# Kernel optimization log

Measured on AMD Instinct MI355X. Metric: run time of the kernel, lower is better.

The kernel has to match this reference:

```python
import jax, jax.numpy as jnp
import numpy as np

NUM_STEPS = 50   # global num_steps in source
SCALE = 1000     # global scale in source (fc1 out / fc2 in)
SUBTHRESH = 0.5  # HeavisideBoxcar surrogate half-width
THRESH = 1.0     # firing threshold

@jax.custom_vjp
def heaviside_boxcar(x):
    # spike = H(x); surrogate grad = boxcar of half-width SUBTHRESH
    return (x >= 0.0).astype(x.dtype)

def _hb_fwd(x):
    return heaviside_boxcar(x), x

def _hb_bwd(x, g):
    return (g * (jnp.abs(x) < SUBTHRESH).astype(g.dtype),)

heaviside_boxcar.defvjp(_hb_fwd, _hb_bwd)


def setup_inputs() -> dict:
    key = jax.random.key(0)
    k1, k2, k3 = jax.random.split(key, 3)
    B = 1024
    x = jax.random.uniform(k1, (B, 784), dtype=jnp.float32)  # pixel intensities in [0,1]
    W1 = jax.random.normal(k2, (SCALE, 784), jnp.float32) / np.sqrt(784).astype(np.float32)
    W2 = jax.random.normal(k3, (100, SCALE), jnp.float32) / np.sqrt(SCALE).astype(np.float32)
    tau_0 = jnp.array([2.0], jnp.float32)       # sigmoid(2) ~ 0.88 decay
    tau_vector = jnp.array([2.0], jnp.float32)
    acc_tau = jnp.array([2.0], jnp.float32)
    return {"x": x, "W1": W1, "W2": W2, "tau_0": tau_0,
            "tau_vector": tau_vector, "acc_tau": acc_tau}


def reference(x, W1, W2, tau_0, tau_vector, acc_tau):
    B = x.shape[0]
    # snn.spikegen.rate: per-step Bernoulli(p=x) spikes, shape [T, B, 784]
    u = jax.random.uniform(jax.random.key(42), (NUM_STEPS, B, 784), dtype=x.dtype)
    x_spk = (u < x[None]).astype(x.dtype)

    decay_0 = jax.nn.sigmoid(tau_0[0])
    decay_v = jax.nn.sigmoid(tau_vector[0])
    acc_decay = jax.nn.sigmoid(acc_tau[0])

    h1_mem = jnp.full((B, SCALE), 0.5, x.dtype)
    h1_spk = jnp.zeros((B, SCALE), x.dtype)
    h2_mem = jnp.full((B, 100), 0.5, x.dtype)
    h2_spk = jnp.zeros((B, 100), x.dtype)
    acc = jnp.zeros((B, 10), x.dtype)

    def step(carry, xt):
        h1m, h1s, h2m, h2s, acc = carry
        # pPLIF: mem = mem*decay*(1-spk) + I ; spike = H(mem - thresh)
        h1m = h1m * decay_0 * (1.0 - h1s) + xt @ W1.T
        h1s = heaviside_boxcar(h1m - THRESH)
        h2m = h2m * decay_v * (1.0 - h2s) + h1s @ W2.T
        h2s = heaviside_boxcar(h2m - THRESH)
        boost = jnp.mean(h2s.reshape(B, 10, 10), axis=2)  # AvgPool1d(10,10)
        acc = acc * acc_decay + boost                      # pPLI accumulator
        return (h1m, h1s, h2m, h2s, acc), None

    carry, _ = jax.lax.scan(step, (h1_mem, h1_spk, h2_mem, h2_spk, acc),
                            x_spk[:NUM_STEPS - 1])
    # torch loop runs under no_grad with detach(): block grads through it
    h1m, h1s, h2m, h2s, acc = jax.tree_util.tree_map(jax.lax.stop_gradient, carry)

    # final, differentiable step
    h1m = h1m * decay_0 * (1.0 - h1s) + x_spk[NUM_STEPS - 1] @ W1.T
    h1s = heaviside_boxcar(h1m - THRESH)
    h2m = h2m * decay_v * (1.0 - h2s) + h1s @ W2.T
    h2s = heaviside_boxcar(h2m - THRESH)
    boost = jnp.mean(h2s.reshape(B, 10, 10), axis=2)
    acc = acc * acc_decay + boost
    return acc
```

## Files before the change

### kernel.cpp

```cpp
#include <hip/hip_runtime.h>
#include <hip/hip_bf16.h>
#include <math.h>


#define NSTEPS 50
#define KC1 25
#define NSL 5

typedef __attribute__((ext_vector_type(4)))  int i32x4;
typedef __attribute__((ext_vector_type(16))) int i32x16;

#define OFF_B1     0ull
#define OFF_B2     5111808ull
#define OFF_H1MST  5898240ull
#define OFF_H1SST  14286848ull
#define OFF_H2MST  15335424ull
#define OFF_H2SST  16384000ull
#define OFF_ACCST  16515072ull
#define OFF_AF     16596992ull
#define FIXED_END  59195392ull
#define PERSTEP    8388608ull

#define PREP_BLOCKS 19200

__device__ __forceinline__ unsigned int rotl32(unsigned int v, int d) {
#if __has_builtin(__builtin_amdgcn_alignbit)
  return __builtin_amdgcn_alignbit(v, v, (unsigned int)(32 - d));
#else
  return (v << d) | (v >> (32 - d));
#endif
}

__device__ __forceinline__ unsigned int tf_bits(unsigned int i) {
  const unsigned int ks0 = 0u;
  const unsigned int ks1 = 42u;
  const unsigned int ks2 = 0x1BD11BDAu ^ 0u ^ 42u;
  unsigned int x0 = 0u + ks0;
  unsigned int x1 = i + ks1;
#define TF_RND(r) { x0 += x1; x1 = rotl32(x1, r); x1 ^= x0; }
  TF_RND(13) TF_RND(15) TF_RND(26) TF_RND(6)
  x0 += ks1; x1 += ks2 + 1u;
  TF_RND(17) TF_RND(29) TF_RND(16) TF_RND(24)
  x0 += ks2; x1 += ks0 + 2u;
  TF_RND(13) TF_RND(15) TF_RND(26) TF_RND(6)
  x0 += ks0; x1 += ks1 + 3u;
  TF_RND(17) TF_RND(29) TF_RND(16) TF_RND(24)
  x0 += ks1; x1 += ks2 + 4u;
  TF_RND(13) TF_RND(15) TF_RND(26) TF_RND(6)
  x0 += ks2; x1 += ks0 + 5u;
#undef TF_RND
  return x0 ^ x1;
}

__device__ __forceinline__ void spike_block(
    const float* __restrict__ x, i32x4* __restrict__ A, int t0, int gblk,
    int tid) {
  int g = gblk * 4 + (tid >> 6);
  int lane = tid & 63;
  int kc = g % 25;
  int r = g / 25;
  int mt = r & 31;
  int t = t0 + (r >> 5);
  int b = mt * 32 + (lane & 31);
  int j0 = kc * 32 + ((lane >> 5) << 4);
  unsigned int wds[4] = {0u, 0u, 0u, 0u};
  if (j0 < 784) {
    unsigned int base = (unsigned int)(t * 1024 + b) * 784u + (unsigned int)j0;
    const float* xp = x + b * 784 + j0;
#pragma unroll
    for (int q = 0; q < 4; ++q) {
      float4 xv = *(const float4*)(xp + 4 * q);
      unsigned int K0 = (unsigned int)(int)ceilf(xv.x * 8388608.0f);
      unsigned int K1 = (unsigned int)(int)ceilf(xv.y * 8388608.0f);
      unsigned int K2 = (unsigned int)(int)ceilf(xv.z * 8388608.0f);
      unsigned int K3 = (unsigned int)(int)ceilf(xv.w * 8388608.0f);
      unsigned int w4 = 0u;
      if ((tf_bits(base + 4 * q + 0) >> 9) < K0) w4 |= 1u;
      if ((tf_bits(base + 4 * q + 1) >> 9) < K1) w4 |= 1u << 8;
      if ((tf_bits(base + 4 * q + 2) >> 9) < K2) w4 |= 1u << 16;
      if ((tf_bits(base + 4 * q + 3) >> 9) < K3) w4 |= 1u << 24;
      wds[q] = w4;
    }
  }
  i32x4 v;
  v.x = (int)wds[0]; v.y = (int)wds[1]; v.z = (int)wds[2]; v.w = (int)wds[3];
  A[(size_t)(((t * 32 + mt) * 26) + kc) * 64 + lane] = v;
}

__global__ __launch_bounds__(256) void setup_kernel(
    const float* __restrict__ W1, const float* __restrict__ W2,
    signed char* __restrict__ B1, signed char* __restrict__ B2,
    const float* __restrict__ x, i32x4* __restrict__ A) {
  if (blockIdx.x >= PREP_BLOCKS) {
    spike_block(x, A, 0, blockIdx.x - PREP_BLOCKS, threadIdx.x);
    return;
  }
  int idx = blockIdx.x * 256 + threadIdx.x;
  const int NB1 = NSL * 32 * 26 * 1024;
  const int NB2 = NSL * 4 * 32 * 1024;
  float w;
  int s;
  signed char* dst;
  if (idx < NB1) {
    int jj = idx & 15;
    int lane = (idx >> 4) & 63;
    int kc = (idx >> 10) % 26;
    int rest = (idx >> 10) / 26;
    int nt = rest & 31;
    s = rest >> 5;
    int k = kc * 32 + ((lane >> 5) << 4) + jj;
    int o = nt * 32 + (lane & 31);
    w = (o < 1000 && k < 784) ? W1[o * 784 + k] : 0.0f;
    dst = B1 + idx;
  } else {
    int m = idx - NB1;
    if (m >= NB2) return;
    int jj = m & 15;
    int lane = (m >> 4) & 63;
    int kc = (m >> 10) & 31;
    int rest = (m >> 10) >> 5;
    int nt = rest & 3;
    s = rest >> 2;
    int k = kc * 32 + ((lane >> 5) << 4) + jj;
    int o = nt * 32 + (lane & 31);
    w = (o < 100 && k < 1000) ? W2[o * 1000 + k] : 0.0f;
    dst = B2 + m;
  }
  long long V = llrint((double)w * 281474976710656.0);
  signed char d = 0;
  for (int q = 0; q <= s + 1; ++q) {
    d = (signed char)(V & 0xFF);
    V = (V - (long long)d) >> 8;
  }
  *dst = d;
}

__global__ __launch_bounds__(256, 2) void gemm1_kernel(
    const signed char* __restrict__ Bf, const signed char* __restrict__ Afc,
    int* __restrict__ T1L, short* __restrict__ T1H) {
  __shared__ i32x4 bls[2][NSL][64];
  int tid = threadIdx.x, lane = tid & 63, wv = tid >> 6;
  int id = blockIdx.x;
  int low5 = id & 31;
  int nt = ((low5 & 7) << 2) | ((low5 >> 3) & 3);
  int mg = id >> 5;
  int tl = mg >> 2;
  int q  = mg & 3;
  int mtA = q * 8 + wv * 2;
  const i32x4* ApA = (const i32x4*)Afc + (size_t)((tl * 32 + mtA) * 26) * 64 + lane;
  const i32x4* ApB = ApA + 26 * 64;
  const i32x4* Bp = (const i32x4*)Bf + lane;
#define B1_IDX(s, kc) ((size_t)(((s) * 32 + nt) * 26 + (kc)) * 64)
  const bool st4 = (wv == 0);

  i32x16 CA[NSL], CB[NSL];
#pragma unroll
  for (int s = 0; s < NSL; ++s)
#pragma unroll
    for (int i = 0; i < 16; ++i) { CA[s][i] = 0; CB[s][i] = 0; }

  i32x4 sa = Bp[B1_IDX(wv, 0)];
  i32x4 sb; if (st4) sb = Bp[B1_IDX(4, 0)];
  i32x4 aA0 = ApA[0], aB0 = ApB[0];
  i32x4 aA1 = ApA[64], aB1 = ApB[64];
  i32x4 aA2, aB2;
  bls[0][wv][lane] = sa;
  if (st4) bls[0][4][lane] = sb;
  sa = Bp[B1_IDX(wv, 1)];
  if (st4) sb = Bp[B1_IDX(4, 1)];
  __syncthreads();

  for (int kc = 0; kc < KC1; ++kc) {
    const int cur = kc & 1, nxt = cur ^ 1;
    if (kc + 1 < KC1) {
      bls[nxt][wv][lane] = sa;
      if (st4) bls[nxt][4][lane] = sb;
    }
    if (kc + 2 < KC1) {
      sa = Bp[B1_IDX(wv, kc + 2)];
      if (st4) sb = Bp[B1_IDX(4, kc + 2)];
      aA2 = ApA[(size_t)(kc + 2) * 64];
      aB2 = ApB[(size_t)(kc + 2) * 64];
    }
#pragma unroll
    for (int s = 0; s < NSL; ++s) {
      i32x4 b = bls[cur][s][lane];
      CA[s] = __builtin_amdgcn_mfma_i32_32x32x32_i8(aA0, b, CA[s], 0, 0, 0);
      CB[s] = __builtin_amdgcn_mfma_i32_32x32x32_i8(aB0, b, CB[s], 0, 0, 0);
    }
    __syncthreads();
    aA0 = aA1; aA1 = aA2;
    aB0 = aB1; aB1 = aB2;
  }

  int o = nt * 32 + (lane & 31);
  int rb = 4 * (lane >> 5);
#pragma unroll
  for (int r = 0; r < 16; ++r) {
    int row = (r & 3) + 8 * (r >> 2) + rb;
    long long TA = (long long)CA[4][r];
    TA = (TA << 8) + (long long)CA[3][r];
    TA = (TA << 8) + (long long)CA[2][r];
    TA = (TA << 8) + (long long)CA[1][r];
    TA = (TA << 8) + (long long)CA[0][r];
    long long TB = (long long)CB[4][r];
    TB = (TB << 8) + (long long)CB[3][r];
    TB = (TB << 8) + (long long)CB[2][r];
    TB = (TB << 8) + (long long)CB[1][r];
    TB = (TB << 8) + (long long)CB[0][r];
    int bA = mtA * 32 + row;
    size_t i0 = ((size_t)tl * 1024 + bA) * 1024 + o;
    size_t i1 = ((size_t)tl * 1024 + bA + 32) * 1024 + o;
    T1L[i0] = (int)TA;
    T1H[i0] = (short)(TA >> 32);
    T1L[i1] = (int)TB;
    T1H[i1] = (short)(TB >> 32);
  }
}

__global__ __launch_bounds__(256) void rec1_kernel(
    const int* __restrict__ T1L, const short* __restrict__ T1H,
    signed char* __restrict__ h1sc,
    double* __restrict__ h1m_st, signed char* __restrict__ h1s_st,
    const float* __restrict__ tau0, int t0, int C,
    const float* __restrict__ x, i32x4* __restrict__ A, int t1) {
  if (blockIdx.x >= 512) {
    spike_block(x, A, t1, blockIdx.x - 512, threadIdx.x);
    return;
  }
  int tid = threadIdx.x;
  int lane = tid & 63, sub = tid >> 6;
  int b = blockIdx.x * 2 + (sub >> 1);
  int obase = (sub & 1) * 512 + lane;
  double alpha = 1.0 / (1.0 + exp(-(double)tau0[0]));
  double m[8], s[8];
  if (t0 == 0) {
#pragma unroll
    for (int j = 0; j < 8; ++j) { m[j] = 0.5; s[j] = 0.0; }
  } else {
#pragma unroll
    for (int j = 0; j < 8; ++j) {
      m[j] = h1m_st[(size_t)b * 1024 + obase + 64 * j];
      s[j] = (double)h1s_st[(size_t)b * 1024 + obase + 64 * j];
    }
  }
  for (int tl = 0; tl < C; ++tl) {
    const int*   Lp = T1L + ((size_t)tl * 1024 + b) * 1024 + obase;
    const short* Hp = T1H + ((size_t)tl * 1024 + b) * 1024 + obase;
    signed char* Sp = h1sc + ((size_t)tl * 1024 + b) * 1024 + obase;
#pragma unroll
    for (int j = 0; j < 8; ++j) {
      long long T = ((long long)Hp[64 * j] << 32) +
                    (long long)(unsigned int)Lp[64 * j];
      double I = (double)T * 0x1p-40;
      m[j] = (s[j] != 0.0 ? 0.0 : m[j] * alpha) + I;
      bool sp = (m[j] - 1.0) >= 0.0;
      s[j] = sp ? 1.0 : 0.0;
      Sp[64 * j] = sp ? 1 : 0;
    }
  }
#pragma unroll
  for (int j = 0; j < 8; ++j) {
    h1m_st[(size_t)b * 1024 + obase + 64 * j] = m[j];
    h1s_st[(size_t)b * 1024 + obase + 64 * j] = (signed char)(s[j] != 0.0 ? 1 : 0);
  }
}

__global__ __launch_bounds__(256, 3) void gemm2_kernel(
    const signed char* __restrict__ Bf, const signed char* __restrict__ h1sc,
    double* __restrict__ T2, int ngemm,
    const float* __restrict__ x, i32x4* __restrict__ A, int t1, int gofs) {
  if ((int)blockIdx.x >= ngemm) {
    spike_block(x, A, t1, gofs + (int)blockIdx.x - ngemm, threadIdx.x);
    return;
  }
  __shared__ i32x4 bls[2][NSL][64];
  int tid = threadIdx.x, lane = tid & 63, wv = tid >> 6;
  int nt = blockIdx.x & 3;
  int mg = blockIdx.x >> 2;
  int tl = mg >> 3;
  int mt = ((mg & 7) << 2) + wv;
  const signed char* Arow =
      h1sc + ((size_t)tl * 1024 + mt * 32 + (lane & 31)) * 1024 + ((lane >> 5) << 4);
  const i32x4* Bp = (const i32x4*)Bf + lane;
  const bool st4 = (wv == 0);
#define B2_IDX(s, kc) ((size_t)(((s) * 4 + nt) * 32 + (kc)) * 64)

  i32x16 C[NSL];
#pragma unroll
  for (int s = 0; s < NSL; ++s)
#pragma unroll
    for (int i = 0; i < 16; ++i) C[s][i] = 0;

  i32x4 sa = Bp[B2_IDX(wv, 0)];
  i32x4 sb; if (st4) sb = Bp[B2_IDX(4, 0)];
  i32x4 a0 = *(const i32x4*)(Arow);
  i32x4 a1 = *(const i32x4*)(Arow + 32);
  i32x4 a2;
  bls[0][wv][lane] = sa;
  if (st4) bls[0][4][lane] = sb;
  sa = Bp[B2_IDX(wv, 1)];
  if (st4) sb = Bp[B2_IDX(4, 1)];
  __syncthreads();

  for (int kc = 0; kc < 32; ++kc) {
    const int cur = kc & 1, nxt = cur ^ 1;
    if (kc + 1 < 32) {
      bls[nxt][wv][lane] = sa;
      if (st4) bls[nxt][4][lane] = sb;
    }
    if (kc + 2 < 32) {
      sa = Bp[B2_IDX(wv, kc + 2)];
      if (st4) sb = Bp[B2_IDX(4, kc + 2)];
      a2 = *(const i32x4*)(Arow + (size_t)(kc + 2) * 32);
    }
    i32x4 b0 = bls[cur][0][lane], b1 = bls[cur][1][lane], b2 = bls[cur][2][lane];
    i32x4 b3 = bls[cur][3][lane], b4 = bls[cur][4][lane];
    C[0] = __builtin_amdgcn_mfma_i32_32x32x32_i8(a0, b0, C[0], 0, 0, 0);
    C[1] = __builtin_amdgcn_mfma_i32_32x32x32_i8(a0, b1, C[1], 0, 0, 0);
    C[2] = __builtin_amdgcn_mfma_i32_32x32x32_i8(a0, b2, C[2], 0, 0, 0);
    C[3] = __builtin_amdgcn_mfma_i32_32x32x32_i8(a0, b3, C[3], 0, 0, 0);
    C[4] = __builtin_amdgcn_mfma_i32_32x32x32_i8(a0, b4, C[4], 0, 0, 0);
    a0 = a1; a1 = a2;
    __syncthreads();
  }

  int o = nt * 32 + (lane & 31);
  int rb = 4 * (lane >> 5);
#pragma unroll
  for (int r = 0; r < 16; ++r) {
    int row = (r & 3) + 8 * (r >> 2) + rb;
    int b = mt * 32 + row;
    long long T = (long long)C[4][r];
    T = (T << 8) + (long long)C[3][r];
    T = (T << 8) + (long long)C[2][r];
    T = (T << 8) + (long long)C[1][r];
    T = (T << 8) + (long long)C[0][r];
    T2[((size_t)tl * 1024 + b) * 128 + o] = (double)T * 0x1p-40;
  }
}

__global__ __launch_bounds__(256) void rec2_kernel(
    const double* __restrict__ T2, double* __restrict__ h2m_st,
    signed char* __restrict__ h2s_st, double* __restrict__ acc_st,
    const float* __restrict__ tauv, const float* __restrict__ acct,
    int t0, int C, float* __restrict__ out) {
  __shared__ signed char sp[256];
  int tid = threadIdx.x;
  int b = blockIdx.x * 2 + (tid >> 7);
  int o = tid & 127;
  double alpha = 1.0 / (1.0 + exp(-(double)tauv[0]));
  double adec  = 1.0 / (1.0 + exp(-(double)acct[0]));
  double m, s, accv = 0.0;
  bool isPool = (o < 10);
  if (t0 == 0) {
    m = 0.5; s = 0.0;
  } else {
    m = h2m_st[(size_t)b * 128 + o];
    s = (double)h2s_st[(size_t)b * 128 + o];
    if (isPool) accv = acc_st[b * 10 + o];
  }
  for (int tl = 0; tl < C; ++tl) {
    double I = T2[((size_t)tl * 1024 + b) * 128 + o];
    m = (s != 0.0 ? 0.0 : m * alpha) + I;
    bool spk = (m - 1.0) >= 0.0;
    s = spk ? 1.0 : 0.0;
    sp[tid] = spk ? 1 : 0;
    __syncthreads();
    if (isPool) {
      int base = tid & 128;
      int isum = 0;
#pragma unroll
      for (int k = 0; k < 10; ++k) isum += sp[base + o * 10 + k];
      accv = accv * adec + (double)isum / 10.0;
      if (t0 + tl == NSTEPS - 1) out[b * 10 + o] = (float)accv;
    }
    __syncthreads();
  }
  h2m_st[(size_t)b * 128 + o] = m;
  h2s_st[(size_t)b * 128 + o] = (signed char)(s != 0.0 ? 1 : 0);
  if (isPool) acc_st[b * 10 + o] = accv;
}

extern "C" void kernel_launch(void* const* d_in, const int* in_sizes, int n_in,
                              void* d_out, int out_size, void* d_ws, size_t ws_size,
                              hipStream_t stream) {
  const float* x    = (const float*)d_in[0];
  const float* W1   = (const float*)d_in[1];
  const float* W2   = (const float*)d_in[2];
  const float* tau0 = (const float*)d_in[3];
  const float* tauv = (const float*)d_in[4];
  const float* acct = (const float*)d_in[5];
  float* out = (float*)d_out;
  char*  ws  = (char*)d_ws;

  signed char* B1     = (signed char*)(ws + OFF_B1);
  signed char* B2     = (signed char*)(ws + OFF_B2);
  double*      h1m_st = (double*)(ws + OFF_H1MST);
  signed char* h1s_st = (signed char*)(ws + OFF_H1SST);
  double*      h2m_st = (double*)(ws + OFF_H2MST);
  signed char* h2s_st = (signed char*)(ws + OFF_H2SST);
  double*      acc_st = (double*)(ws + OFF_ACCST);
  signed char* Af     = (signed char*)(ws + OFF_AF);
  i32x4*       Afv    = (i32x4*)Af;

  long long avail = (long long)ws_size - (long long)FIXED_END;
  int C = (int)(avail / (long long)PERSTEP);
  if (C < 1) C = 1;
  if (C > 13) C = 13;
  size_t off_t1l  = FIXED_END;
  size_t off_t1h  = off_t1l + (size_t)C * 4194304ull;
  size_t off_h1sc = off_t1h + (size_t)C * 2097152ull;
  size_t off_t2   = off_h1sc + (size_t)C * 1048576ull;
  int*         T1L  = (int*)(ws + off_t1l);
  short*       T1H  = (short*)(ws + off_t1h);
  signed char* h1sc = (signed char*)(ws + off_h1sc);
  double*      T2   = (double*)(ws + off_t2);

  int C0 = (C < NSTEPS) ? C : NSTEPS;
  setup_kernel<<<PREP_BLOCKS + C0 * 200, 256, 0, stream>>>(
      W1, W2, B1, B2, x, Afv);

  for (int t0 = 0; t0 < NSTEPS; t0 += C) {
    int Cc = (NSTEPS - t0 < C) ? (NSTEPS - t0) : C;
    int t1 = t0 + Cc;
    int Cn = (t1 < NSTEPS) ? ((NSTEPS - t1 < C) ? (NSTEPS - t1) : C) : 0;
    int spkTot = Cn * 200;
    int spkA = spkTot / 2;
    int spkB = spkTot - spkA;
    int ngemm2 = 4 * Cc * 8;

    gemm1_kernel<<<32 * Cc * 4, 256, 0, stream>>>(
        B1, Af + (size_t)t0 * 851968ull, T1L, T1H);
    rec1_kernel<<<512 + spkA, 256, 0, stream>>>(
        T1L, T1H, h1sc, h1m_st, h1s_st, tau0, t0, Cc, x, Afv, t1);
    gemm2_kernel<<<ngemm2 + spkB, 256, 0, stream>>>(
        B2, h1sc, T2, ngemm2, x, Afv, t1, spkA);
    rec2_kernel<<<512, 256, 0, stream>>>(
        T2, h2m_st, h2s_st, acc_st, tauv, acct, t0, Cc, out);
  }
}
```

Measured before the change: 484.6 us.

## Preload whole W1 tile into LDS and drop per-chunk barriers in gemm1

Reorders the packed B1 weight layout so that each output tile's slices and k-chunks are contiguous. gemm1 then copies the whole 25x5 chunk set for its tile into shared memory (about 125 KB) once at the start. The main k-loop has no barriers or double-buffer stores, and A-operand prefetch now runs three chunks ahead. The larger LDS footprint forces occupancy down to one block per CU (launch bounds changed to 1), and the upfront bulk load is no longer overlapped with MFMA work.

```diff
diff --git a/kernel.cpp b/kernel.cpp
--- a/kernel.cpp
+++ b/kernel.cpp
@@ -104,10 +104,10 @@
   if (idx < NB1) {
     int jj = idx & 15;
     int lane = (idx >> 4) & 63;
-    int kc = (idx >> 10) % 26;
-    int rest = (idx >> 10) / 26;
-    int nt = rest & 31;
-    s = rest >> 5;
+    int fr = idx >> 10;
+    s = fr % 5;
+    int kc = (fr / 5) % 26;
+    int nt = fr / (5 * 26);
     int k = kc * 32 + ((lane >> 5) << 4) + jj;
     int o = nt * 32 + (lane & 31);
     w = (o < 1000 && k < 784) ? W1[o * 784 + k] : 0.0f;
@@ -135,10 +135,10 @@
   *dst = d;
 }
 
-__global__ __launch_bounds__(256, 2) void gemm1_kernel(
+__global__ __launch_bounds__(256, 1) void gemm1_kernel(
     const signed char* __restrict__ Bf, const signed char* __restrict__ Afc,
     int* __restrict__ T1L, short* __restrict__ T1H) {
-  __shared__ i32x4 bls[2][NSL][64];
+  __shared__ i32x4 bls[KC1 * NSL * 64];
   int tid = threadIdx.x, lane = tid & 63, wv = tid >> 6;
   int id = blockIdx.x;
   int low5 = id & 31;
@@ -147,11 +147,16 @@
   int tl = mg >> 2;
   int q  = mg & 3;
   int mtA = q * 8 + wv * 2;
+
+  const i32x4* Bg = (const i32x4*)Bf + (size_t)nt * (26 * NSL * 64);
+#pragma unroll
+  for (int i = 0; i < 32; ++i) {
+    int e = tid + 256 * i;
+    if (e < KC1 * NSL * 64) bls[e] = Bg[e];
+  }
+
   const i32x4* ApA = (const i32x4*)Afc + (size_t)((tl * 32 + mtA) * 26) * 64 + lane;
   const i32x4* ApB = ApA + 26 * 64;
-  const i32x4* Bp = (const i32x4*)Bf + lane;
-#define B1_IDX(s, kc) ((size_t)(((s) * 32 + nt) * 26 + (kc)) * 64)
-  const bool st4 = (wv == 0);
 
   i32x16 CA[NSL], CB[NSL];
 #pragma unroll
@@ -159,38 +164,26 @@
 #pragma unroll
     for (int i = 0; i < 16; ++i) { CA[s][i] = 0; CB[s][i] = 0; }
 
-  i32x4 sa = Bp[B1_IDX(wv, 0)];
-  i32x4 sb; if (st4) sb = Bp[B1_IDX(4, 0)];
-  i32x4 aA0 = ApA[0], aB0 = ApB[0];
-  i32x4 aA1 = ApA[64], aB1 = ApB[64];
-  i32x4 aA2, aB2;
-  bls[0][wv][lane] = sa;
-  if (st4) bls[0][4][lane] = sb;
-  sa = Bp[B1_IDX(wv, 1)];
-  if (st4) sb = Bp[B1_IDX(4, 1)];
   __syncthreads();
 
+  i32x4 aA0 = ApA[0],   aB0 = ApB[0];
+  i32x4 aA1 = ApA[64],  aB1 = ApB[64];
+  i32x4 aA2 = ApA[128], aB2 = ApB[128];
+
   for (int kc = 0; kc < KC1; ++kc) {
-    const int cur = kc & 1, nxt = cur ^ 1;
-    if (kc + 1 < KC1) {
-      bls[nxt][wv][lane] = sa;
-      if (st4) bls[nxt][4][lane] = sb;
-    }
-    if (kc + 2 < KC1) {
-      sa = Bp[B1_IDX(wv, kc + 2)];
-      if (st4) sb = Bp[B1_IDX(4, kc + 2)];
-      aA2 = ApA[(size_t)(kc + 2) * 64];
-      aB2 = ApB[(size_t)(kc + 2) * 64];
-    }
-#pragma unroll
-    for (int s = 0; s < NSL; ++s) {
-      i32x4 b = bls[cur][s][lane];
-      CA[s] = __builtin_amdgcn_mfma_i32_32x32x32_i8(aA0, b, CA[s], 0, 0, 0);
-      CB[s] = __builtin_amdgcn_mfma_i32_32x32x32_i8(aB0, b, CB[s], 0, 0, 0);
-    }
-    __syncthreads();
+    i32x4 ua = aA0, ub = aB0;
     aA0 = aA1; aA1 = aA2;
     aB0 = aB1; aB1 = aB2;
+    if (kc + 3 < KC1) {
+      aA2 = ApA[(size_t)(kc + 3) * 64];
+      aB2 = ApB[(size_t)(kc + 3) * 64];
+    }
+#pragma unroll
+    for (int s = 0; s < NSL; ++s) {
+      i32x4 b = bls[(kc * NSL + s) * 64 + lane];
+      CA[s] = __builtin_amdgcn_mfma_i32_32x32x32_i8(ua, b, CA[s], 0, 0, 0);
+      CB[s] = __builtin_amdgcn_mfma_i32_32x32x32_i8(ub, b, CB[s], 0, 0, 0);
+    }
   }
 
   int o = nt * 32 + (lane & 31);
```

After: 625.6 us. 29.1% more time.
